# Optimization experiments

Measured on AMD Instinct MI355X. Metric: run time of the kernel, lower is better.

## Reference

```python
import jax, jax.numpy as jnp
import numpy as np

N_NODES = 40000
N_EDGES = 640000
HIDDEN = 128


def setup_inputs() -> dict:
    key = jax.random.key(0)
    k_h, k_w, k_b, k_src, k_dst = jax.random.split(key, 5)
    h = jax.random.normal(k_h, (N_NODES, HIDDEN), dtype=jnp.float32)
    # nn.Linear(hidden_dim, hidden_dim): weight [out, in], bias [out]
    W = jax.random.normal(k_w, (HIDDEN, HIDDEN), dtype=jnp.float32) * (1.0 / np.sqrt(HIDDEN))
    b = jax.random.normal(k_b, (HIDDEN,), dtype=jnp.float32) * 0.01
    src = jax.random.randint(k_src, (N_EDGES,), 0, N_NODES, dtype=jnp.int32)
    dst = jax.random.randint(k_dst, (N_EDGES,), 0, N_NODES, dtype=jnp.int32)
    return {"h": h, "W": W, "b": b, "src": src, "dst": dst}


def reference(h, W, b, src, dst):
    n = h.shape[0]
    # message: gather source node features; reduce: mailbox sum == segment-sum by dst
    agg = jax.ops.segment_sum(h[src], dst, num_segments=n)  # [N, D]
    updated = agg @ W.T + b  # merge_linner
    # DGL update_all only writes nodes with >=1 incoming edge; others keep old h
    indeg = jax.ops.segment_sum(jnp.ones(src.shape, dtype=h.dtype), dst, num_segments=n)
    return jnp.where((indeg > 0)[:, None], updated, h)
```

## Files before the change

### kernel.cpp

```cpp
#include <hip/hip_runtime.h>
#include <hip/hip_bf16.h>

static constexpr int HIDDEN = 128;

using bf16x8 = __attribute__((ext_vector_type(8))) __bf16;
using f32x4 = __attribute__((ext_vector_type(4))) float;
using ushort8v = __attribute__((ext_vector_type(8))) ushort;

__device__ inline ushort f2bf(float x) {
  __hip_bfloat16 t = __float2bfloat16(x);
  return *reinterpret_cast<ushort*>(&t);
}

__global__ void __launch_bounds__(256) wconv_kernel(
    const float* __restrict__ W, ushort* __restrict__ wbf) {
  int i = (blockIdx.x * 256 + threadIdx.x) * 4;
  if (i < HIDDEN * HIDDEN) {
    float4 w = *reinterpret_cast<const float4*>(W + i);
    ushort4 u;
    u.x = f2bf(w.x);
    u.y = f2bf(w.y);
    u.z = f2bf(w.z);
    u.w = f2bf(w.w);
    *reinterpret_cast<ushort4*>(wbf + i) = u;
  }
}

__global__ void __launch_bounds__(256) hist_transform_kernel(
    const int* __restrict__ dst, int* __restrict__ counts, int n_edges,
    int nbh, const float* __restrict__ h, const ushort* __restrict__ wbf,
    ushort* __restrict__ hW, int n_nodes) {
  constexpr int COLP = 136;
  __shared__ ushort tile[4][16][COLP];

  if (blockIdx.x < nbh) {
    int i = blockIdx.x * 256 + threadIdx.x;
    if (i < n_edges) atomicAdd(&counts[dst[i]], 1);
    return;
  }

  const int tb = blockIdx.x - nbh;
  const int wave = threadIdx.x >> 6;
  const int lane = threadIdx.x & 63;
  const int r16 = lane & 15;
  const int kq = lane >> 4;
  const int kbase = kq * 8;
  const int base = tb * 64 + wave * 16;

  int arow = base + r16;
  if (arow >= n_nodes) arow = n_nodes - 1;
  const float* hrow = h + (size_t)arow * HIDDEN;

  bf16x8 a[4];
#pragma unroll
  for (int ks = 0; ks < 4; ++ks) {
    const float4 u = *reinterpret_cast<const float4*>(hrow + ks * 32 + kbase);
    const float4 v =
        *reinterpret_cast<const float4*>(hrow + ks * 32 + kbase + 4);
    bf16x8 t;
    t[0] = (__bf16)u.x;
    t[1] = (__bf16)u.y;
    t[2] = (__bf16)u.z;
    t[3] = (__bf16)u.w;
    t[4] = (__bf16)v.x;
    t[5] = (__bf16)v.y;
    t[6] = (__bf16)v.z;
    t[7] = (__bf16)v.w;
    a[ks] = t;
  }

#pragma unroll
  for (int ct = 0; ct < 8; ++ct) {
    const ushort* wrow = wbf + (size_t)(ct * 16 + r16) * HIDDEN;
    f32x4 acc = {0.f, 0.f, 0.f, 0.f};
#pragma unroll
    for (int ks = 0; ks < 4; ++ks) {
      bf16x8 bfrag = *reinterpret_cast<const bf16x8*>(wrow + ks * 32 + kbase);
      acc = __builtin_amdgcn_mfma_f32_16x16x32_bf16(a[ks], bfrag, acc, 0, 0, 0);
    }
#pragma unroll
    for (int r = 0; r < 4; ++r)
      tile[wave][kq * 4 + r][ct * 16 + r16] = f2bf(acc[r]);
  }
#pragma unroll
  for (int it = 0; it < 4; ++it) {
    const int row = it * 4 + (lane >> 4);
    const int cb = r16 * 8;
    const int nrow = base + row;
    if (nrow < n_nodes) {
      ushort8v v = *reinterpret_cast<const ushort8v*>(&tile[wave][row][cb]);
      *reinterpret_cast<ushort8v*>(hW + (size_t)nrow * HIDDEN + cb) = v;
    }
  }
}

__global__ void __launch_bounds__(256) scanA_kernel(
    const int* __restrict__ counts, int* __restrict__ tilesums, int n) {
  const int t = threadIdx.x;
  const int base = blockIdx.x * 1024 + t * 4;
  int s = 0;
  if (base + 3 < n) {
    int4 v = *reinterpret_cast<const int4*>(counts + base);
    s = v.x + v.y + v.z + v.w;
  } else {
    for (int j = 0; j < 4; ++j)
      if (base + j < n) s += counts[base + j];
  }
  for (int off = 1; off < 64; off <<= 1) s += __shfl_xor(s, off, 64);
  __shared__ int wp[4];
  if ((t & 63) == 0) wp[t >> 6] = s;
  __syncthreads();
  if (t == 0) tilesums[blockIdx.x] = wp[0] + wp[1] + wp[2] + wp[3];
}

__global__ void __launch_bounds__(256) scanC_kernel(
    const int* __restrict__ counts, const int* __restrict__ tilesums,
    int* __restrict__ offsets, int n, int nt) {
  __shared__ int tp[64];
  const int t = threadIdx.x;
  if (t < 64) {
    int v = (t < nt) ? tilesums[t] : 0;
    int orig = v;
    for (int off = 1; off < 64; off <<= 1) {
      int u = __shfl_up(v, off, 64);
      if (t >= off) v += u;
    }
    tp[t] = v - orig;
  }
  __syncthreads();

  const int base = blockIdx.x * 1024 + t * 4;
  int4 v = {0, 0, 0, 0};
  const bool full = (base + 3 < n);
  if (full) {
    v = *reinterpret_cast<const int4*>(counts + base);
  } else {
    if (base + 0 < n) v.x = counts[base + 0];
    if (base + 1 < n) v.y = counts[base + 1];
    if (base + 2 < n) v.z = counts[base + 2];
    if (base + 3 < n) v.w = counts[base + 3];
  }
  const int s = v.x + v.y + v.z + v.w;
  int inc = s;
  for (int off = 1; off < 64; off <<= 1) {
    int u = __shfl_up(inc, off, 64);
    if ((t & 63) >= off) inc += u;
  }
  const int excl = inc - s;
  __shared__ int wp[4];
  if ((t & 63) == 63) wp[t >> 6] = inc;
  __syncthreads();
  int wbase = 0;
  for (int w = 0; w < (t >> 6); ++w) wbase += wp[w];
  int p = tp[blockIdx.x] + wbase + excl;
  if (full) {
    int4 o;
    o.x = p;
    o.y = p + v.x;
    o.z = p + v.x + v.y;
    o.w = p + v.x + v.y + v.z;
    *reinterpret_cast<int4*>(offsets + base) = o;
  } else {
    int run = p;
    if (base + 0 < n) { offsets[base + 0] = run; run += v.x; }
    if (base + 1 < n) { offsets[base + 1] = run; run += v.y; }
    if (base + 2 < n) { offsets[base + 2] = run; run += v.z; }
    if (base + 3 < n) { offsets[base + 3] = run; }
  }
}

__global__ void __launch_bounds__(256) fill_kernel(
    const int* __restrict__ src, const int* __restrict__ dst,
    int* __restrict__ offsets, int* __restrict__ esorted, int n_edges) {
  int i = blockIdx.x * 256 + threadIdx.x;
  if (i < n_edges) {
    int pos = atomicAdd(&offsets[dst[i]], 1);
    esorted[pos] = src[i];
  }
}

__global__ void __launch_bounds__(256) gather_sum_kernel(
    const ushort* __restrict__ hW, const float* __restrict__ h,
    const float* __restrict__ b, const int* __restrict__ counts,
    const int* __restrict__ ends, const int* __restrict__ esorted,
    float* __restrict__ out, int n_nodes) {
  const int lane = threadIdx.x & 7;
  const int group = threadIdx.x >> 3;
  const int f0 = lane * 16;
  const int node = blockIdx.x * 32 + group;
  if (node >= n_nodes) return;

  const int deg = counts[node];
  f32x4 A = {0.f, 0.f, 0.f, 0.f};
  f32x4 B = {0.f, 0.f, 0.f, 0.f};
  f32x4 C = {0.f, 0.f, 0.f, 0.f};
  f32x4 D = {0.f, 0.f, 0.f, 0.f};
  if (deg == 0) {
    const float* hr = h + (size_t)node * HIDDEN + f0;
    float4 t0 = *reinterpret_cast<const float4*>(hr + 0);
    float4 t1 = *reinterpret_cast<const float4*>(hr + 4);
    float4 t2 = *reinterpret_cast<const float4*>(hr + 8);
    float4 t3 = *reinterpret_cast<const float4*>(hr + 12);
    A = {t0.x, t0.y, t0.z, t0.w};
    B = {t1.x, t1.y, t1.z, t1.w};
    C = {t2.x, t2.y, t2.z, t2.w};
    D = {t3.x, t3.y, t3.z, t3.w};
  } else {
    const int start = ends[node] - deg;
    for (int base = 0; base < deg; base += 8) {
      int sreg = 0;
      if (base + lane < deg)
        sreg = __builtin_nontemporal_load(esorted + start + base + lane);
      const int m = min(8, deg - base);
#pragma unroll 8
      for (int jj = 0; jj < m; ++jj) {
        int s = __shfl(sreg, jj, 8);
        const uint4* rp =
            reinterpret_cast<const uint4*>(hW + (size_t)s * HIDDEN + f0);
        uint4 v0 = rp[0];
        uint4 v1 = rp[1];
        A[0] += __uint_as_float(v0.x << 16);
        A[1] += __uint_as_float(v0.x & 0xffff0000u);
        A[2] += __uint_as_float(v0.y << 16);
        A[3] += __uint_as_float(v0.y & 0xffff0000u);
        B[0] += __uint_as_float(v0.z << 16);
        B[1] += __uint_as_float(v0.z & 0xffff0000u);
        B[2] += __uint_as_float(v0.w << 16);
        B[3] += __uint_as_float(v0.w & 0xffff0000u);
        C[0] += __uint_as_float(v1.x << 16);
        C[1] += __uint_as_float(v1.x & 0xffff0000u);
        C[2] += __uint_as_float(v1.y << 16);
        C[3] += __uint_as_float(v1.y & 0xffff0000u);
        D[0] += __uint_as_float(v1.z << 16);
        D[1] += __uint_as_float(v1.z & 0xffff0000u);
        D[2] += __uint_as_float(v1.w << 16);
        D[3] += __uint_as_float(v1.w & 0xffff0000u);
      }
    }
    const float4 b0 = *reinterpret_cast<const float4*>(b + f0 + 0);
    const float4 b1 = *reinterpret_cast<const float4*>(b + f0 + 4);
    const float4 b2 = *reinterpret_cast<const float4*>(b + f0 + 8);
    const float4 b3 = *reinterpret_cast<const float4*>(b + f0 + 12);
    A[0] += b0.x; A[1] += b0.y; A[2] += b0.z; A[3] += b0.w;
    B[0] += b1.x; B[1] += b1.y; B[2] += b1.z; B[3] += b1.w;
    C[0] += b2.x; C[1] += b2.y; C[2] += b2.z; C[3] += b2.w;
    D[0] += b3.x; D[1] += b3.y; D[2] += b3.z; D[3] += b3.w;
  }
  float* op = out + (size_t)node * HIDDEN + f0;
  __builtin_nontemporal_store(A, reinterpret_cast<f32x4*>(op + 0));
  __builtin_nontemporal_store(B, reinterpret_cast<f32x4*>(op + 4));
  __builtin_nontemporal_store(C, reinterpret_cast<f32x4*>(op + 8));
  __builtin_nontemporal_store(D, reinterpret_cast<f32x4*>(op + 12));
}


__global__ void __launch_bounds__(256) hist_kernel(
    const int* __restrict__ dst, int* __restrict__ counts, int n_edges) {
  int i = blockIdx.x * 256 + threadIdx.x;
  if (i < n_edges) atomicAdd(&counts[dst[i]], 1);
}

__global__ void __launch_bounds__(1024) scan_kernel(
    const int* __restrict__ counts, int* __restrict__ offsets, int n) {
  __shared__ int part[1024];
  const int t = threadIdx.x;
  const int C = (n + 1023) / 1024;
  const int base = t * C;
  int sum = 0;
  for (int j = 0; j < C; ++j) {
    int idx = base + j;
    if (idx < n) sum += counts[idx];
  }
  part[t] = sum;
  __syncthreads();
  for (int s = 1; s < 1024; s <<= 1) {
    int v = (t >= s) ? part[t - s] : 0;
    __syncthreads();
    part[t] += v;
    __syncthreads();
  }
  int run = part[t] - sum;
  for (int j = 0; j < C; ++j) {
    int idx = base + j;
    if (idx < n) {
      offsets[idx] = run;
      run += counts[idx];
    }
  }
}

__global__ void __launch_bounds__(256, 2) gather_update_kernel(
    const float* __restrict__ h, const float* __restrict__ W,
    const float* __restrict__ b, const int* __restrict__ counts,
    const int* __restrict__ ends, const int* __restrict__ esorted,
    float* __restrict__ out, int n_nodes) {
  __shared__ float Wt[HIDDEN][HIDDEN];
  for (int i = threadIdx.x; i < HIDDEN * HIDDEN / 4; i += 256) {
    int idx = i * 4;
    int j = idx >> 7;
    int k = idx & 127;
    float4 w = *reinterpret_cast<const float4*>(W + j * HIDDEN + k);
    Wt[k + 0][j] = w.x;
    Wt[k + 1][j] = w.y;
    Wt[k + 2][j] = w.z;
    Wt[k + 3][j] = w.w;
  }
  __syncthreads();
  const int lane = threadIdx.x & 31;
  const int group = threadIdx.x >> 5;
  const int j0 = lane * 4;
  const float4 bias = *reinterpret_cast<const float4*>(b + j0);
  const int nb = (n_nodes + 7) >> 3;
  for (int batch = blockIdx.x; batch < nb; batch += gridDim.x) {
    int node = batch * 8 + group;
    if (node >= n_nodes) continue;
    const int deg = counts[node];
    float4 res;
    if (deg == 0) {
      res = reinterpret_cast<const float4*>(h + (size_t)node * HIDDEN)[lane];
    } else {
      const int start = ends[node] - deg;
      float4 acc = {0.f, 0.f, 0.f, 0.f};
      for (int basei = 0; basei < deg; basei += 32) {
        int sreg = 0;
        if (basei + lane < deg) sreg = esorted[start + basei + lane];
        const int m = min(32, deg - basei);
        for (int jj = 0; jj < m; ++jj) {
          int s = __shfl(sreg, jj, 32);
          float4 v =
              reinterpret_cast<const float4*>(h + (size_t)s * HIDDEN)[lane];
          acc.x += v.x;
          acc.y += v.y;
          acc.z += v.z;
          acc.w += v.w;
        }
      }
      const float* av = reinterpret_cast<const float*>(&acc);
      float4 o = bias;
#pragma unroll
      for (int k = 0; k < HIDDEN; ++k) {
        float aval = __shfl(av[k & 3], k >> 2, 32);
        float4 w = *reinterpret_cast<const float4*>(&Wt[k][j0]);
        o.x = fmaf(aval, w.x, o.x);
        o.y = fmaf(aval, w.y, o.y);
        o.z = fmaf(aval, w.z, o.z);
        o.w = fmaf(aval, w.w, o.w);
      }
      res = o;
    }
    reinterpret_cast<float4*>(out + (size_t)node * HIDDEN)[lane] = res;
  }
}


extern "C" void kernel_launch(void* const* d_in, const int* in_sizes, int n_in,
                              void* d_out, int out_size, void* d_ws, size_t ws_size,
                              hipStream_t stream) {
  const float* h = (const float*)d_in[0];
  const float* W = (const float*)d_in[1];
  const float* b = (const float*)d_in[2];
  const int* src = (const int*)d_in[3];
  const int* dst = (const int*)d_in[4];
  float* out = (float*)d_out;
  const int n_nodes = in_sizes[0] / HIDDEN;
  const int n_edges = in_sizes[3];

  const int n_round = (n_nodes + 1023) & ~1023;
  const int nt = n_round / 1024;
  const int eblocks1 = (n_edges + 255) / 256;

  int* counts = (int*)d_ws;
  int* offsets = counts + n_round;
  int* tilesums = offsets + n_round;
  int* esorted = tilesums + 64;
  size_t off_bytes = ((size_t)(2 * n_round + 64 + n_edges) * 4 + 15) & ~15ull;
  ushort* hW = (ushort*)((char*)d_ws + off_bytes);
  size_t wbf_off = (off_bytes + (size_t)n_nodes * HIDDEN * 2 + 15) & ~15ull;
  ushort* wbf = (ushort*)((char*)d_ws + wbf_off);
  const size_t need_full = wbf_off + (size_t)HIDDEN * HIDDEN * 2;

  if (ws_size >= need_full && nt <= 64) {
    (void)hipMemsetAsync(counts, 0, (size_t)n_nodes * sizeof(int), stream);
    wconv_kernel<<<(HIDDEN * HIDDEN / 4 + 255) / 256, 256, 0, stream>>>(W,
                                                                        wbf);
    const int tblocks = (n_nodes + 63) / 64;
    hist_transform_kernel<<<eblocks1 + tblocks, 256, 0, stream>>>(
        dst, counts, n_edges, eblocks1, h, wbf, hW, n_nodes);
    scanA_kernel<<<nt, 256, 0, stream>>>(counts, tilesums, n_nodes);
    scanC_kernel<<<nt, 256, 0, stream>>>(counts, tilesums, offsets, n_nodes,
                                         nt);
    fill_kernel<<<eblocks1, 256, 0, stream>>>(src, dst, offsets, esorted,
                                              n_edges);
    const int gblocks = (n_nodes + 31) / 32;
    gather_sum_kernel<<<gblocks, 256, 0, stream>>>(hW, h, b, counts, offsets,
                                                   esorted, out, n_nodes);
  } else {
    (void)hipMemsetAsync(counts, 0, (size_t)n_nodes * sizeof(int), stream);
    hist_kernel<<<eblocks1, 256, 0, stream>>>(dst, counts, n_edges);
    scan_kernel<<<1, 1024, 0, stream>>>(counts, offsets, n_nodes);
    fill_kernel<<<eblocks1, 256, 0, stream>>>(src, dst, offsets, esorted,
                                              n_edges);
    gather_update_kernel<<<512, 256, 0, stream>>>(h, W, b, counts, offsets,
                                                  esorted, out, n_nodes);
  }
}
```

Baseline: 184.3 us.

## Record per-edge rank in histogram to make CSR fill atomic-free

The histogram pass now saves the value returned by each atomicAdd as a per-edge rank, so the fill pass can place edges at offsets[dst]+rank without a second round of atomics. The fill is vectorised to four edges per thread. The W conversion is merged into the histogram launch, and the MFMA transform is split back out into its own kernel that runs after the fill. The trade is an extra 640K-int rank array written and read, plus losing the overlap between the histogram and the transform.

```diff
diff --git a/kernel.cpp b/kernel.cpp
--- a/kernel.cpp
+++ b/kernel.cpp
@@ -12,40 +12,132 @@
   return *reinterpret_cast<ushort*>(&t);
 }
 
-__global__ void __launch_bounds__(256) wconv_kernel(
+__global__ void __launch_bounds__(256) hist_rank_wconv_kernel(
+    const int* __restrict__ dst, int* __restrict__ counts,
+    int* __restrict__ rank, int n_edges, int nbh,
     const float* __restrict__ W, ushort* __restrict__ wbf) {
+  if (blockIdx.x < nbh) {
+    int i = blockIdx.x * 256 + threadIdx.x;
+    if (i < n_edges) rank[i] = atomicAdd(&counts[dst[i]], 1);
+  } else {
+    int i = ((blockIdx.x - nbh) * 256 + threadIdx.x) * 4;
+    if (i < HIDDEN * HIDDEN) {
+      float4 w = *reinterpret_cast<const float4*>(W + i);
+      ushort4 u;
+      u.x = f2bf(w.x);
+      u.y = f2bf(w.y);
+      u.z = f2bf(w.z);
+      u.w = f2bf(w.w);
+      *reinterpret_cast<ushort4*>(wbf + i) = u;
+    }
+  }
+}
+
+__global__ void __launch_bounds__(256) scanA_kernel(
+    const int* __restrict__ counts, int* __restrict__ tilesums, int n) {
+  const int t = threadIdx.x;
+  const int base = blockIdx.x * 1024 + t * 4;
+  int s = 0;
+  if (base + 3 < n) {
+    int4 v = *reinterpret_cast<const int4*>(counts + base);
+    s = v.x + v.y + v.z + v.w;
+  } else {
+    for (int j = 0; j < 4; ++j)
+      if (base + j < n) s += counts[base + j];
+  }
+  for (int off = 1; off < 64; off <<= 1) s += __shfl_xor(s, off, 64);
+  __shared__ int wp[4];
+  if ((t & 63) == 0) wp[t >> 6] = s;
+  __syncthreads();
+  if (t == 0) tilesums[blockIdx.x] = wp[0] + wp[1] + wp[2] + wp[3];
+}
+
+__global__ void __launch_bounds__(256) scanC_kernel(
+    const int* __restrict__ counts, const int* __restrict__ tilesums,
+    int* __restrict__ offsets, int n, int nt) {
+  __shared__ int tp[64];
+  const int t = threadIdx.x;
+  if (t < 64) {
+    int v = (t < nt) ? tilesums[t] : 0;
+    int orig = v;
+    for (int off = 1; off < 64; off <<= 1) {
+      int u = __shfl_up(v, off, 64);
+      if (t >= off) v += u;
+    }
+    tp[t] = v - orig;
+  }
+  __syncthreads();
+
+  const int base = blockIdx.x * 1024 + t * 4;
+  int4 v = {0, 0, 0, 0};
+  const bool full = (base + 3 < n);
+  if (full) {
+    v = *reinterpret_cast<const int4*>(counts + base);
+  } else {
+    if (base + 0 < n) v.x = counts[base + 0];
+    if (base + 1 < n) v.y = counts[base + 1];
+    if (base + 2 < n) v.z = counts[base + 2];
+    if (base + 3 < n) v.w = counts[base + 3];
+  }
+  const int s = v.x + v.y + v.z + v.w;
+  int inc = s;
+  for (int off = 1; off < 64; off <<= 1) {
+    int u = __shfl_up(inc, off, 64);
+    if ((t & 63) >= off) inc += u;
+  }
+  const int excl = inc - s;
+  __shared__ int wp[4];
+  if ((t & 63) == 63) wp[t >> 6] = inc;
+  __syncthreads();
+  int wbase = 0;
+  for (int w = 0; w < (t >> 6); ++w) wbase += wp[w];
+  int p = tp[blockIdx.x] + wbase + excl;
+  if (full) {
+    int4 o;
+    o.x = p;
+    o.y = p + v.x;
+    o.z = p + v.x + v.y;
+    o.w = p + v.x + v.y + v.z;
+    *reinterpret_cast<int4*>(offsets + base) = o;
+  } else {
+    int run = p;
+    if (base + 0 < n) { offsets[base + 0] = run; run += v.x; }
+    if (base + 1 < n) { offsets[base + 1] = run; run += v.y; }
+    if (base + 2 < n) { offsets[base + 2] = run; run += v.z; }
+    if (base + 3 < n) { offsets[base + 3] = run; }
+  }
+}
+
+__global__ void __launch_bounds__(256) fill_scatter_kernel(
+    const int* __restrict__ src, const int* __restrict__ dst,
+    const int* __restrict__ offsets, const int* __restrict__ rank,
+    int* __restrict__ esorted, int n_edges) {
   int i = (blockIdx.x * 256 + threadIdx.x) * 4;
-  if (i < HIDDEN * HIDDEN) {
-    float4 w = *reinterpret_cast<const float4*>(W + i);
-    ushort4 u;
-    u.x = f2bf(w.x);
-    u.y = f2bf(w.y);
-    u.z = f2bf(w.z);
-    u.w = f2bf(w.w);
-    *reinterpret_cast<ushort4*>(wbf + i) = u;
-  }
-}
-
-__global__ void __launch_bounds__(256) hist_transform_kernel(
-    const int* __restrict__ dst, int* __restrict__ counts, int n_edges,
-    int nbh, const float* __restrict__ h, const ushort* __restrict__ wbf,
+  if (i + 3 < n_edges) {
+    int4 s = *reinterpret_cast<const int4*>(src + i);
+    int4 d = *reinterpret_cast<const int4*>(dst + i);
+    int4 r = *reinterpret_cast<const int4*>(rank + i);
+    esorted[offsets[d.x] + r.x] = s.x;
+    esorted[offsets[d.y] + r.y] = s.y;
+    esorted[offsets[d.z] + r.z] = s.z;
+    esorted[offsets[d.w] + r.w] = s.w;
+  } else {
+    for (int j = i; j < n_edges; ++j)
+      esorted[offsets[dst[j]] + rank[j]] = src[j];
+  }
+}
+
+__global__ void __launch_bounds__(256) transform_mfma_kernel(
+    const float* __restrict__ h, const ushort* __restrict__ wbf,
     ushort* __restrict__ hW, int n_nodes) {
   constexpr int COLP = 136;
   __shared__ ushort tile[4][16][COLP];
-
-  if (blockIdx.x < nbh) {
-    int i = blockIdx.x * 256 + threadIdx.x;
-    if (i < n_edges) atomicAdd(&counts[dst[i]], 1);
-    return;
-  }
-
-  const int tb = blockIdx.x - nbh;
   const int wave = threadIdx.x >> 6;
   const int lane = threadIdx.x & 63;
   const int r16 = lane & 15;
   const int kq = lane >> 4;
   const int kbase = kq * 8;
-  const int base = tb * 64 + wave * 16;
+  const int base = blockIdx.x * 64 + wave * 16;
 
   int arow = base + r16;
   if (arow >= n_nodes) arow = n_nodes - 1;
@@ -94,95 +186,10 @@
   }
 }
 
-__global__ void __launch_bounds__(256) scanA_kernel(
-    const int* __restrict__ counts, int* __restrict__ tilesums, int n) {
-  const int t = threadIdx.x;
-  const int base = blockIdx.x * 1024 + t * 4;
-  int s = 0;
-  if (base + 3 < n) {
-    int4 v = *reinterpret_cast<const int4*>(counts + base);
-    s = v.x + v.y + v.z + v.w;
-  } else {
-    for (int j = 0; j < 4; ++j)
-      if (base + j < n) s += counts[base + j];
-  }
-  for (int off = 1; off < 64; off <<= 1) s += __shfl_xor(s, off, 64);
-  __shared__ int wp[4];
-  if ((t & 63) == 0) wp[t >> 6] = s;
-  __syncthreads();
-  if (t == 0) tilesums[blockIdx.x] = wp[0] + wp[1] + wp[2] + wp[3];
-}
-
-__global__ void __launch_bounds__(256) scanC_kernel(
-    const int* __restrict__ counts, const int* __restrict__ tilesums,
-    int* __restrict__ offsets, int n, int nt) {
-  __shared__ int tp[64];
-  const int t = threadIdx.x;
-  if (t < 64) {
-    int v = (t < nt) ? tilesums[t] : 0;
-    int orig = v;
-    for (int off = 1; off < 64; off <<= 1) {
-      int u = __shfl_up(v, off, 64);
-      if (t >= off) v += u;
-    }
-    tp[t] = v - orig;
-  }
-  __syncthreads();
-
-  const int base = blockIdx.x * 1024 + t * 4;
-  int4 v = {0, 0, 0, 0};
-  const bool full = (base + 3 < n);
-  if (full) {
-    v = *reinterpret_cast<const int4*>(counts + base);
-  } else {
-    if (base + 0 < n) v.x = counts[base + 0];
-    if (base + 1 < n) v.y = counts[base + 1];
-    if (base + 2 < n) v.z = counts[base + 2];
-    if (base + 3 < n) v.w = counts[base + 3];
-  }
-  const int s = v.x + v.y + v.z + v.w;
-  int inc = s;
-  for (int off = 1; off < 64; off <<= 1) {
-    int u = __shfl_up(inc, off, 64);
-    if ((t & 63) >= off) inc += u;
-  }
-  const int excl = inc - s;
-  __shared__ int wp[4];
-  if ((t & 63) == 63) wp[t >> 6] = inc;
-  __syncthreads();
-  int wbase = 0;
-  for (int w = 0; w < (t >> 6); ++w) wbase += wp[w];
-  int p = tp[blockIdx.x] + wbase + excl;
-  if (full) {
-    int4 o;
-    o.x = p;
-    o.y = p + v.x;
-    o.z = p + v.x + v.y;
-    o.w = p + v.x + v.y + v.z;
-    *reinterpret_cast<int4*>(offsets + base) = o;
-  } else {
-    int run = p;
-    if (base + 0 < n) { offsets[base + 0] = run; run += v.x; }
-    if (base + 1 < n) { offsets[base + 1] = run; run += v.y; }
-    if (base + 2 < n) { offsets[base + 2] = run; run += v.z; }
-    if (base + 3 < n) { offsets[base + 3] = run; }
-  }
-}
-
-__global__ void __launch_bounds__(256) fill_kernel(
-    const int* __restrict__ src, const int* __restrict__ dst,
-    int* __restrict__ offsets, int* __restrict__ esorted, int n_edges) {
-  int i = blockIdx.x * 256 + threadIdx.x;
-  if (i < n_edges) {
-    int pos = atomicAdd(&offsets[dst[i]], 1);
-    esorted[pos] = src[i];
-  }
-}
-
 __global__ void __launch_bounds__(256) gather_sum_kernel(
     const ushort* __restrict__ hW, const float* __restrict__ h,
     const float* __restrict__ b, const int* __restrict__ counts,
-    const int* __restrict__ ends, const int* __restrict__ esorted,
+    const int* __restrict__ starts, const int* __restrict__ esorted,
     float* __restrict__ out, int n_nodes) {
   const int lane = threadIdx.x & 7;
   const int group = threadIdx.x >> 3;
@@ -206,7 +213,7 @@
     C = {t2.x, t2.y, t2.z, t2.w};
     D = {t3.x, t3.y, t3.z, t3.w};
   } else {
-    const int start = ends[node] - deg;
+    const int start = starts[node];
     for (int base = 0; base < deg; base += 8) {
       int sreg = 0;
       if (base + lane < deg)
@@ -258,6 +265,16 @@
     const int* __restrict__ dst, int* __restrict__ counts, int n_edges) {
   int i = blockIdx.x * 256 + threadIdx.x;
   if (i < n_edges) atomicAdd(&counts[dst[i]], 1);
+}
+
+__global__ void __launch_bounds__(256) fill_atomic_kernel(
+    const int* __restrict__ src, const int* __restrict__ dst,
+    int* __restrict__ offsets, int* __restrict__ esorted, int n_edges) {
+  int i = blockIdx.x * 256 + threadIdx.x;
+  if (i < n_edges) {
+    int pos = atomicAdd(&offsets[dst[i]], 1);
+    esorted[pos] = src[i];
+  }
 }
 
 __global__ void __launch_bounds__(1024) scan_kernel(
@@ -368,12 +385,15 @@
   const int n_round = (n_nodes + 1023) & ~1023;
   const int nt = n_round / 1024;
   const int eblocks1 = (n_edges + 255) / 256;
+  const int eblocks4 = (n_edges + 1023) / 1024;
 
   int* counts = (int*)d_ws;
   int* offsets = counts + n_round;
   int* tilesums = offsets + n_round;
   int* esorted = tilesums + 64;
-  size_t off_bytes = ((size_t)(2 * n_round + 64 + n_edges) * 4 + 15) & ~15ull;
+  int* rank = esorted + n_edges;
+  size_t off_bytes =
+      ((size_t)(2 * n_round + 64 + 2 * n_edges) * 4 + 15) & ~15ull;
   ushort* hW = (ushort*)((char*)d_ws + off_bytes);
   size_t wbf_off = (off_bytes + (size_t)n_nodes * HIDDEN * 2 + 15) & ~15ull;
   ushort* wbf = (ushort*)((char*)d_ws + wbf_off);
@@ -381,16 +401,16 @@
 
   if (ws_size >= need_full && nt <= 64) {
     (void)hipMemsetAsync(counts, 0, (size_t)n_nodes * sizeof(int), stream);
-    wconv_kernel<<<(HIDDEN * HIDDEN / 4 + 255) / 256, 256, 0, stream>>>(W,
-                                                                        wbf);
-    const int tblocks = (n_nodes + 63) / 64;
-    hist_transform_kernel<<<eblocks1 + tblocks, 256, 0, stream>>>(
-        dst, counts, n_edges, eblocks1, h, wbf, hW, n_nodes);
+    const int wblocks = (HIDDEN * HIDDEN / 4 + 255) / 256;
+    hist_rank_wconv_kernel<<<eblocks1 + wblocks, 256, 0, stream>>>(
+        dst, counts, rank, n_edges, eblocks1, W, wbf);
     scanA_kernel<<<nt, 256, 0, stream>>>(counts, tilesums, n_nodes);
     scanC_kernel<<<nt, 256, 0, stream>>>(counts, tilesums, offsets, n_nodes,
                                          nt);
-    fill_kernel<<<eblocks1, 256, 0, stream>>>(src, dst, offsets, esorted,
-                                              n_edges);
+    fill_scatter_kernel<<<eblocks4, 256, 0, stream>>>(src, dst, offsets, rank,
+                                                      esorted, n_edges);
+    const int tblocks = (n_nodes + 63) / 64;
+    transform_mfma_kernel<<<tblocks, 256, 0, stream>>>(h, wbf, hW, n_nodes);
     const int gblocks = (n_nodes + 31) / 32;
     gather_sum_kernel<<<gblocks, 256, 0, stream>>>(hW, h, b, counts, offsets,
                                                    esorted, out, n_nodes);
@@ -398,8 +418,8 @@
     (void)hipMemsetAsync(counts, 0, (size_t)n_nodes * sizeof(int), stream);
     hist_kernel<<<eblocks1, 256, 0, stream>>>(dst, counts, n_edges);
     scan_kernel<<<1, 1024, 0, stream>>>(counts, offsets, n_nodes);
-    fill_kernel<<<eblocks1, 256, 0, stream>>>(src, dst, offsets, esorted,
-                                              n_edges);
+    fill_atomic_kernel<<<eblocks1, 256, 0, stream>>>(src, dst, offsets,
+                                                     esorted, n_edges);
     gather_update_kernel<<<512, 256, 0, stream>>>(h, W, b, counts, offsets,
                                                   esorted, out, n_nodes);
   }
```

Measured after the change: 162.7 us. -11.8%, faster.
